# Performance work log

Hardware: AMD Instinct MI355X
Metric: run time of the kernel (lower is better)

Reference implementation:

```python
import jax, jax.numpy as jnp
import numpy as np

B, S1, S2, H, DW = 64, 512, 512, 768, 200


def setup_inputs() -> dict:
    key = jax.random.key(0)
    ks = jax.random.split(key, 16)
    inp = {
        'x1': jax.random.normal(ks[0], (B, S1, H), jnp.float32),
        'x1_h': jax.random.normal(ks[1], (B, H), jnp.float32),
        'x1_mask': jax.random.randint(ks[2], (B, S1), 0, 2, jnp.int32),
        'y': jax.random.normal(ks[3], (B, S1), jnp.float32),
        'x2': jax.random.normal(ks[4], (B, S2, H), jnp.float32),
        'x2_h': jax.random.normal(ks[5], (B, H), jnp.float32),
        'x2_mask': jax.random.randint(ks[6], (B, S2), 0, 2, jnp.int32),
        'tt': jax.random.normal(ks[7], (B, S1, DW), jnp.float32),
        'tt2': jax.random.normal(ks[8], (B, S2, DW), jnp.float32),
        # parameters (xavier ~ N(0, 2/(fan_in+fan_out)))
        'W_bert': jax.random.normal(ks[9], (H + 1, H), jnp.float32) * np.sqrt(2.0 / (H + 1 + H)),
        'W_wv': jax.random.normal(ks[10], (DW + 1, DW), jnp.float32) * np.sqrt(2.0 / (DW + 1 + DW)),
        'lin_wv_w': jax.random.normal(ks[11], (DW, H), jnp.float32) * np.sqrt(1.0 / DW),
        'lin_wv_b': jnp.zeros((H,), jnp.float32),
        'lin_w': jax.random.normal(ks[12], (4 * H, 1), jnp.float32) * np.sqrt(1.0 / (4 * H)),
        'lin_b': jnp.zeros((1,), jnp.float32),
    }
    return inp


def _branch(x_cat, W, keys_vals, x1_inv, x2_inv):
    # x_cat: [B,S1,D+1], W: [D+1,D], keys_vals: [B,S2,D]
    xw = jnp.matmul(x_cat, W)                                  # [B,S1,D]
    a = jnp.einsum('bsd,btd->bst', xw, keys_vals)              # [B,S1,S2]
    a = jnp.where(x2_inv[:, None, :], jnp.float32(-1e-5), a)   # faithful: tiny mask value, pre-softmax
    a = jax.nn.softmax(a, axis=-1)
    v = jnp.einsum('bst,btd->bsd', a, keys_vals)               # [B,S1,D]
    v = jnp.where(x1_inv[:, :, None], jnp.float32(-1e5), v)
    return v.max(axis=1)                                       # max-pool over S1 -> [B,D]


def reference(x1, x1_h, x1_mask, y, x2, x2_h, x2_mask, tt, tt2,
              W_bert, W_wv, lin_wv_w, lin_wv_b, lin_w, lin_b):
    x1_inv = (1 - x1_mask).astype(bool)  # True where padded
    x2_inv = (1 - x2_mask).astype(bool)

    # word-vector branch
    x1_wv = jnp.concatenate([tt, y[:, :, None]], axis=-1)      # [B,S1,201]
    x12_wv = _branch(x1_wv, W_wv, tt2, x1_inv, x2_inv)         # [B,200]
    x12_wv = x12_wv @ lin_wv_w + lin_wv_b                      # [B,768]

    # bert branch
    x1c = jnp.concatenate([x1, y[:, :, None]], axis=-1)        # [B,S1,769]
    x12 = _branch(x1c, W_bert, x2, x1_inv, x2_inv)             # [B,768]

    h = jnp.concatenate([x1_h, x2_h, x12, x12_wv], axis=1)     # [B,3072]
    o = jax.nn.sigmoid(h @ lin_w + lin_b)                      # [B,1]
    return (o, x1_inv.astype(jnp.int32), x2_inv.astype(jnp.int32))
```

## Files before the change

### kernel.cpp

```cpp
#include <hip/hip_runtime.h>


#define BB 64
#define SS 512
#define HH 768
#define DWW 200

typedef __attribute__((ext_vector_type(8))) _Float16 f16x8;
typedef __attribute__((ext_vector_type(4))) _Float16 f16x4;
typedef __attribute__((ext_vector_type(4))) float f32x4;
typedef unsigned int u32;

__device__ __forceinline__ u32 fkey(float f) {
    u32 u = __float_as_uint(f);
    return (u & 0x80000000u) ? ~u : (u | 0x80000000u);
}
__device__ __forceinline__ float fdec(u32 k) {
    u32 u = (k & 0x80000000u) ? (k & 0x7fffffffu) : ~k;
    return __uint_as_float(u);
}
__device__ __forceinline__ f32x4 mm(f16x8 a, f16x8 b, f32x4 c) {
    return __builtin_amdgcn_mfma_f32_16x16x32_f16(a, b, c, 0, 0, 0);
}
__device__ __forceinline__ void gl16(const void* g, void* l) {
    __builtin_amdgcn_global_load_lds(
        (const __attribute__((address_space(1))) void*)g,
        (__attribute__((address_space(3))) void*)l, 16, 0, 0);
}

__global__ __launch_bounds__(256) void k_setup(
    const int* __restrict__ m1, const int* __restrict__ m2,
    const float* __restrict__ Wb, const float* __restrict__ Wwv,
    float* __restrict__ out, u32* __restrict__ k1, u32* __restrict__ k2,
    int* __restrict__ idx1, int* __restrict__ rcnt1,
    int* __restrict__ idx2, int* __restrict__ rcnt2,
    _Float16* __restrict__ wbTH, _Float16* __restrict__ wwTH) {
    int bid = blockIdx.x, tid = threadIdx.x;
    if (bid < 128) {
        int i = bid * 256 + tid;
        out[BB + i]           = (float)(1 - m1[i]);
        out[BB + BB * SS + i] = (float)(1 - m2[i]);
    } else if (bid < 320) {
        int i = (bid - 128) * 256 + tid;
        u32 v = fkey(-1e5f);
        if (i < BB * HH) k1[i] = v;
        if (i < BB * DWW) k2[i] = v;
    } else if (bid < 448) {
        int b = (bid - 320) & 63;
        const int* m = (bid < 384) ? m1 : m2;
        int* idx = (bid < 384) ? idx1 : idx2;
        int* rcnt = (bid < 384) ? rcnt1 : rcnt2;
        if (tid < 64) {
            int base = 0;
#pragma unroll
            for (int c = 0; c < 8; ++c) {
                int s = c * 64 + tid;
                int v = m[b * SS + s];
                unsigned long long bal = __ballot(v != 0);
                int pre = __popcll(bal & ((1ull << tid) - 1ull));
                if (v) idx[b * SS + base + pre] = s;
                base += __popcll(bal);
            }
            if (tid == 0) rcnt[b] = base;
        }
    } else if (bid < 2848) {
        int i = (bid - 448) * 256 + tid;
        int n = i / 800, k = i - n * 800;
        wbTH[i] = (_Float16)((k < 769) ? Wb[(size_t)k * 768 + n] : 0.f);
    } else {
        int i = (bid - 2848) * 256 + tid;
        int n = i / 224, k = i - n * 224;
        wwTH[i] = (_Float16)((k < 201 && n < 200) ? Wwv[(size_t)k * 200 + n] : 0.f);
    }
}

__global__ __launch_bounds__(256) void k_prep(
    const float* __restrict__ x2, const float* __restrict__ tt2,
    const float* __restrict__ x1, const float* __restrict__ tt,
    const float* __restrict__ yv,
    const int* __restrict__ idx1, const int* __restrict__ rcnt1,
    const int* __restrict__ idx2, const int* __restrict__ rcnt2,
    _Float16* __restrict__ kvB, _Float16* __restrict__ kvTB,
    _Float16* __restrict__ kvW, _Float16* __restrict__ kvTW,
    _Float16* __restrict__ XcB, _Float16* __restrict__ XcW,
    int cb, int b0) {
    __shared__ float tile[64][65];
    int bx = blockIdx.x, tid = threadIdx.x;
    if (bx < cb * 128) {
        int cbi = bx >> 7, sub = bx & 127;
        int t0 = (sub & 7) * 64, ybr = sub >> 3;
        const float* src; _Float16* kv; _Float16* kvT; int D, DPAD, DTPAD, d0;
        if (ybr < 12) { src = x2;  kv = kvB; kvT = kvTB; D = 768; DPAD = 768; DTPAD = 768; d0 = ybr * 64; }
        else          { src = tt2; kv = kvW; kvT = kvTW; D = 200; DPAD = 256; DTPAD = 256; d0 = (ybr - 12) * 64; }
        int bg = b0 + cbi;
        int rc2 = rcnt2[bg];
        int tpad2 = (rc2 + 127) & ~127;
        if (t0 >= tpad2) return;
        int tq = tid >> 3, c8 = (tid & 7) * 8;
#pragma unroll
        for (int i = 0; i < 2; ++i) {
            int t = tq + i * 32;
            int tg = t0 + t;
            int gd = d0 + c8;
            float v[8] = {0.f, 0.f, 0.f, 0.f, 0.f, 0.f, 0.f, 0.f};
            if (tg < rc2) {
                int sg = idx2[bg * SS + tg];
                const float* rp = src + ((size_t)bg * SS + sg) * D + gd;
                if (gd + 7 < D) {
                    float4 p0 = *(const float4*)(rp);
                    float4 p1 = *(const float4*)(rp + 4);
                    v[0] = p0.x; v[1] = p0.y; v[2] = p0.z; v[3] = p0.w;
                    v[4] = p1.x; v[5] = p1.y; v[6] = p1.z; v[7] = p1.w;
                } else {
#pragma unroll
                    for (int j = 0; j < 8; ++j) {
                        int d = gd + j;
                        v[j] = (d < D) ? src[((size_t)bg * SS + sg) * D + d] : 0.f;
                    }
                }
            }
            f16x8 o;
#pragma unroll
            for (int j = 0; j < 8; ++j) {
                tile[t][c8 + j] = v[j];
                o[j] = (_Float16)v[j];
            }
            *(f16x8*)(kv + ((size_t)cbi * SS + tg) * DPAD + gd) = o;
        }
        __syncthreads();
#pragma unroll
        for (int i = 0; i < 2; ++i) {
            int dl = tq + i * 32, gdr = d0 + dl;
            if (gdr < DTPAD) {
                f16x8 o;
#pragma unroll
                for (int j = 0; j < 8; ++j) o[j] = (_Float16)tile[c8 + j][dl];
                *(f16x8*)(kvT + ((size_t)cbi * DTPAD + gdr) * SS + t0 + c8) = o;
            }
        }
    } else {
        bx -= cb * 128;
        int cbi = bx >> 8, xb = bx & 255;
        int bg = b0 + cbi;
        const float* X; _Float16* outp; int Din, KPAD; size_t ost;
        if (xb < 200) { X = x1; outp = XcB; Din = 768; KPAD = 800; ost = (size_t)cbi * 409600; }
        else { xb -= 200; X = tt; outp = XcW; Din = 200; KPAD = 224; ost = (size_t)cbi * 114688; }
        int i8 = (xb * 256 + tid) * 8;
        int s = i8 / KPAD, k0 = i8 - s * KPAD;
        int rc = rcnt1[bg];
        int rpad = (rc + 127) & ~127;
        if (s >= rpad) return;
        f16x8 o = {};
        if (s < rc) {
            int sg = idx1[bg * SS + s];
            const float* Xr = X + ((size_t)bg * SS + sg) * Din;
            if (k0 + 7 < Din) {
                float4 p0 = *(const float4*)(Xr + k0);
                float4 p1 = *(const float4*)(Xr + k0 + 4);
                o[0] = (_Float16)p0.x; o[1] = (_Float16)p0.y;
                o[2] = (_Float16)p0.z; o[3] = (_Float16)p0.w;
                o[4] = (_Float16)p1.x; o[5] = (_Float16)p1.y;
                o[6] = (_Float16)p1.z; o[7] = (_Float16)p1.w;
            } else {
#pragma unroll
                for (int j = 0; j < 8; ++j) {
                    int k = k0 + j;
                    float v = (k < Din) ? Xr[k]
                                        : ((k == Din) ? yv[(size_t)bg * SS + sg] : 0.f);
                    o[j] = (_Float16)v;
                }
            }
        }
        *(f16x8*)(outp + ost + (size_t)s * KPAD + k0) = o;
    }
}

template<int KA, int KST, int TN, int SXW, int DV, int AS, int BS, int EPI,
         bool GN, bool RK>
__device__ __forceinline__ void mm_core(
    const _Float16* __restrict__ A, const _Float16* __restrict__ B,
    _Float16* __restrict__ O, const float* __restrict__ rsum,
    u32* __restrict__ keys, int jb, const int* __restrict__ rcnt1,
    const int* __restrict__ rcnt2, int b0, char* lds, float* rsv) {
    int cbi = jb / (4 * TN);
    int rest = jb - cbi * (4 * TN);
    int ts = rest / TN, tn = rest - ts * TN;
    int s0 = ts * 128, n0 = tn * 128;

    int rc = rcnt1[b0 + cbi];
    int rpad = (rc + 127) & ~127;
    if (s0 >= rpad) return;
    if constexpr (GN) {
        int tp2 = (rcnt2[b0 + cbi] + 127) & ~127;
        if (n0 >= tp2) return;
    }

    int tid = threadIdx.x, lane = tid & 63, wid = tid >> 6;
    int wr = wid >> 1, wc = wid & 1;
    int l15 = lane & 15, sl = lane >> 4, gb = sl * 4;

    const _Float16* srcA = A + (size_t)cbi * AS + (size_t)s0 * KA;
    const _Float16* srcB = B + (size_t)cbi * BS + (size_t)n0 * KA;

    if constexpr (EPI == 2) {
        if (tid < 128) rsv[tid] = rsum[cbi * SS + s0 + tid];
    }

    f32x4 zz = {0.f, 0.f, 0.f, 0.f};
    f32x4 acc[4][4];
#pragma unroll
    for (int i = 0; i < 4; ++i)
#pragma unroll
        for (int j = 0; j < 4; ++j) acc[i][j] = zz;

#define STAGE(buf, ks)                                                        \
    _Pragma("unroll") for (int i = 0; i < 4; ++i) {                           \
        int c = wid + 4 * i;                                                  \
        int arr = c >> 3, sub = c & 7, slot = sub >> 1, rh = sub & 1;         \
        const _Float16* gp = (arr ? srcB : srcA) +                            \
            (size_t)(rh * 64 + lane) * KA + (ks) * 32 + slot * 8;             \
        gl16(gp, lds + (buf) * 16384 + c * 1024);                             \
    }
#define KBODY(ks, kend)                                                       \
    {                                                                         \
        if ((ks) + 1 < (kend)) STAGE(buf ^ 1, (ks) + 1);                      \
        char* base = lds + buf * 16384;                                       \
        f16x8 a[4], b[4];                                                     \
        _Pragma("unroll") for (int mf = 0; mf < 4; ++mf)                      \
            a[mf] = *(const f16x8*)(base + sl * 2048 +                        \
                                    (wr * 64 + mf * 16 + l15) * 16);          \
        _Pragma("unroll") for (int nf = 0; nf < 4; ++nf)                      \
            b[nf] = *(const f16x8*)(base + 8192 + sl * 2048 +                 \
                                    (wc * 64 + nf * 16 + l15) * 16);          \
        _Pragma("unroll") for (int mf = 0; mf < 4; ++mf)                      \
            _Pragma("unroll") for (int nf = 0; nf < 4; ++nf)                  \
                acc[mf][nf] = mm(a[mf], b[nf], acc[mf][nf]);                  \
        __syncthreads();                                                      \
        buf ^= 1;                                                             \
    }

    STAGE(0, 0);
    __syncthreads();
    int buf = 0;
    if constexpr (RK) {
        int kend = ((rcnt2[b0 + cbi] + 127) & ~127) >> 5;
        for (int ks = 0; ks < kend; ++ks) KBODY(ks, kend);
    } else {
#pragma unroll
        for (int ks = 0; ks < KST; ++ks) KBODY(ks, KST);
    }
#undef KBODY
#undef STAGE

    if constexpr (EPI == 1) {
        _Float16* ce = (_Float16*)lds;
#pragma unroll
        for (int mf = 0; mf < 4; ++mf)
#pragma unroll
            for (int nf = 0; nf < 4; ++nf)
#pragma unroll
                for (int r = 0; r < 4; ++r) {
                    int row = wr * 64 + mf * 16 + gb + r;
                    int col = wc * 64 + nf * 16 + l15;
                    ce[row * 128 + col] = (_Float16)acc[mf][nf][r];
                }
        __syncthreads();
#pragma unroll
        for (int i = 0; i < 8; ++i) {
            int t = tid + i * 256;
            int row = t >> 4, col = (t & 15) * 8;
            *(f16x8*)(O + ((size_t)cbi * SS + s0 + row) * SXW + n0 + col) =
                *(const f16x8*)(ce + row * 128 + col);
        }
    } else {
        int bg = b0 + cbi;
#pragma unroll
        for (int nf = 0; nf < 4; ++nf) {
            float mx = -3.0e38f;
#pragma unroll
            for (int mf = 0; mf < 4; ++mf)
#pragma unroll
                for (int r = 0; r < 4; ++r) {
                    int srow = wr * 64 + mf * 16 + gb + r;
                    if (s0 + srow < rc) mx = fmaxf(mx, acc[mf][nf][r] * rsv[srow]);
                }
            mx = fmaxf(mx, __shfl_xor(mx, 16));
            mx = fmaxf(mx, __shfl_xor(mx, 32));
            if (lane < 16) {
                int d = n0 + wc * 64 + nf * 16 + lane;
                if (d < DV) atomicMax(&keys[(size_t)bg * DV + d], fkey(mx));
            }
        }
    }
}

template<int EPI, bool GN, bool RK,
         int KA0, int KST0, int TN0, int SXW0, int DV0, int AS0, int BS0,
         int KA1, int KST1, int TN1, int SXW1, int DV1, int AS1, int BS1>
__global__ __launch_bounds__(256) void k_mmM(
    const _Float16* __restrict__ A0, const _Float16* __restrict__ B0,
    _Float16* __restrict__ O0, const float* __restrict__ rs0, u32* __restrict__ key0,
    const _Float16* __restrict__ A1, const _Float16* __restrict__ B1,
    _Float16* __restrict__ O1, const float* __restrict__ rs1, u32* __restrict__ key1,
    int nj0, const int* __restrict__ rcnt1, const int* __restrict__ rcnt2,
    int b0, int nwg) {
    __shared__ __align__(16) char lds[32768];
    __shared__ float rsv[128];
    int bid = blockIdx.x;
    int x = bid & 7, t = bid >> 3;
    int tb = nj0 >> 3;
    int tw = (nwg - nj0) >> 3;
    if (t < tb)
        mm_core<KA0, KST0, TN0, SXW0, DV0, AS0, BS0, EPI, GN, RK>(
            A0, B0, O0, rs0, key0, x * tb + t, rcnt1, rcnt2, b0, lds, rsv);
    else
        mm_core<KA1, KST1, TN1, SXW1, DV1, AS1, BS1, EPI, GN, RK>(
            A1, B1, O1, rs1, key1, x * tw + (t - tb), rcnt1, rcnt2, b0, lds, rsv);
}

__global__ __launch_bounds__(256) void k_softmaxM(
    _Float16* __restrict__ SP0, float* __restrict__ rs0,
    _Float16* __restrict__ SP1, float* __restrict__ rs1,
    const int* __restrict__ rcnt1, const int* __restrict__ rcnt2,
    int nblk0, int b0) {
    int bid = blockIdx.x;
    bool selw = bid >= nblk0;
    int b = selw ? bid - nblk0 : bid;
    _Float16* SP = selw ? SP1 : SP0;
    float* rs = selw ? rs1 : rs0;
    int cbi = b >> 7, rb = b & 127;
    int wid = threadIdx.x >> 6, lane = threadIdx.x & 63;
    int row = rb * 4 + wid, bg = b0 + cbi;
    int rc1 = rcnt1[bg];
    if (row >= rc1) return;
    int rc2 = rcnt2[bg];
    int col0 = lane * 8;
    f16x8 sv = *(const f16x8*)(SP + ((size_t)cbi * SS + row) * SS + col0);
    float mx = -3.0e38f;
    float c[8];
#pragma unroll
    for (int j = 0; j < 8; ++j) {
        c[j] = (float)sv[j];
        if (col0 + j < rc2) mx = fmaxf(mx, c[j]);
    }
#pragma unroll
    for (int off = 1; off <= 32; off <<= 1) mx = fmaxf(mx, __shfl_xor(mx, off));
    f16x8 o;
    float sm = 0.f;
#pragma unroll
    for (int j = 0; j < 8; ++j) {
        _Float16 h = (col0 + j < rc2) ? (_Float16)__expf(c[j] - mx) : (_Float16)0.f;
        o[j] = h;
        sm += (float)h;
    }
#pragma unroll
    for (int off = 1; off <= 32; off <<= 1) sm += __shfl_xor(sm, off);
    *(f16x8*)(SP + ((size_t)cbi * SS + row) * SS + col0) = o;
    if (lane == 0) rs[cbi * SS + row] = 1.0f / sm;
}

__global__ __launch_bounds__(256) void k_tail(
    const float* __restrict__ x1h, const float* __restrict__ x2h,
    const u32* __restrict__ keys, const u32* __restrict__ wvkeys,
    const float* __restrict__ Wp, const float* __restrict__ bp,
    const float* __restrict__ lw, const float* __restrict__ lb,
    float* __restrict__ out) {
    int b = blockIdx.x, tid = threadIdx.x;
    __shared__ float xv[DWW];
    __shared__ float wvp[HH];
    __shared__ float red[4];
    if (tid < DWW) xv[tid] = fdec(wvkeys[b * DWW + tid]);
    __syncthreads();
    for (int h = tid; h < HH; h += 256) {
        float acc = bp[h];
        for (int d = 0; d < DWW; ++d) acc += xv[d] * Wp[d * HH + h];
        wvp[h] = acc;
    }
    __syncthreads();
    float acc = 0.f;
    for (int i = tid; i < HH; i += 256) {
        acc += x1h[b * HH + i] * lw[i];
        acc += x2h[b * HH + i] * lw[HH + i];
        acc += fdec(keys[b * HH + i]) * lw[2 * HH + i];
        acc += wvp[i] * lw[3 * HH + i];
    }
    int wid = tid >> 6, lane = tid & 63;
#pragma unroll
    for (int off = 32; off; off >>= 1) acc += __shfl_down(acc, off);
    if (lane == 0) red[wid] = acc;
    __syncthreads();
    if (tid == 0) {
        float z = red[0] + red[1] + red[2] + red[3] + lb[0];
        out[b] = 1.f / (1.f + __expf(-z));
    }
}

extern "C" void kernel_launch(void* const* d_in, const int* in_sizes, int n_in,
                              void* d_out, int out_size, void* d_ws, size_t ws_size,
                              hipStream_t stream) {
    const float* x1   = (const float*)d_in[0];
    const float* x1h  = (const float*)d_in[1];
    const int*   m1   = (const int*)d_in[2];
    const float* y    = (const float*)d_in[3];
    const float* x2   = (const float*)d_in[4];
    const float* x2h  = (const float*)d_in[5];
    const int*   m2   = (const int*)d_in[6];
    const float* tt   = (const float*)d_in[7];
    const float* tt2  = (const float*)d_in[8];
    const float* Wb   = (const float*)d_in[9];
    const float* Wwv  = (const float*)d_in[10];
    const float* lwvw = (const float*)d_in[11];
    const float* lwvb = (const float*)d_in[12];
    const float* lw   = (const float*)d_in[13];
    const float* lb   = (const float*)d_in[14];
    float* out = (float*)d_out;
    char* ws = (char*)d_ws;

    u32*      x12key   = (u32*)ws;
    u32*      x12wvkey = (u32*)(ws + 196608);
    float*    rsumB    = (float*)(ws + 444416);
    float*    rsumW    = (float*)(ws + 575488);
    _Float16* wbTH     = (_Float16*)(ws + 706560);
    _Float16* wwTH     = (_Float16*)(ws + 1935360);
    int*      idx1Buf  = (int*)(ws + 2050048);
    int*      rcnt1Buf = (int*)(ws + 2181120);
    int*      idx2Buf  = (int*)(ws + 2181376);
    int*      rcnt2Buf = (int*)(ws + 2312448);
    const size_t D0 = 2312704;

    k_setup<<<3072, 256, 0, stream>>>(m1, m2, Wb, Wwv, out, x12key, x12wvkey,
                                      idx1Buf, rcnt1Buf, idx2Buf, rcnt2Buf,
                                      wbTH, wwTH);

    const size_t perb = 4194304;
    int nb = 1;
    if (ws_size > D0 + perb) nb = (int)((ws_size - D0) / perb);
    if (nb > BB) nb = BB;
    if (nb < 1) nb = 1;

    char* R = ws + D0;
    _Float16* XcB = (_Float16*)R;
    _Float16* XcW = (_Float16*)(R + (size_t)nb * 819200);
    _Float16* S_b = (_Float16*)R;
    _Float16* S_w = (_Float16*)(R + (size_t)nb * 524288);
    char* p = R + (size_t)nb * 1048576;
    _Float16* XW_b = (_Float16*)p; p += (size_t)nb * 786432;
    _Float16* XW_w = (_Float16*)p; p += (size_t)nb * 262144;
    _Float16* KV_b = (_Float16*)p; p += (size_t)nb * 786432;
    _Float16* KV_w = (_Float16*)p; p += (size_t)nb * 262144;
    _Float16* KT_b = (_Float16*)p; p += (size_t)nb * 786432;
    _Float16* KT_w = (_Float16*)p;

    for (int b0 = 0; b0 < BB; b0 += nb) {
        int cb = (BB - b0 < nb) ? (BB - b0) : nb;
        k_prep<<<cb * 384, 256, 0, stream>>>(
            x2, tt2, x1, tt, y, idx1Buf, rcnt1Buf, idx2Buf, rcnt2Buf,
            KV_b, KT_b, KV_w, KT_w, XcB, XcW, cb, b0);
        k_mmM<1, false, false,
              800, 25, 6, 768, 0, 409600, 0,
              224,  7, 2, 256, 0, 114688, 0><<<cb * 32, 256, 0, stream>>>(
            XcB, wbTH, XW_b, nullptr, nullptr,
            XcW, wwTH, XW_w, nullptr, nullptr,
            cb * 24, rcnt1Buf, rcnt2Buf, b0, cb * 32);
        k_mmM<1, true, false,
              768, 24, 4, 512, 0, 393216, 393216,
              256,  8, 4, 512, 0, 131072, 131072><<<cb * 32, 256, 0, stream>>>(
            XW_b, KV_b, S_b, nullptr, nullptr,
            XW_w, KV_w, S_w, nullptr, nullptr,
            cb * 16, rcnt1Buf, rcnt2Buf, b0, cb * 32);
        k_softmaxM<<<cb * 256, 256, 0, stream>>>(
            S_b, rsumB, S_w, rsumW, rcnt1Buf, rcnt2Buf, cb * 128, b0);
        k_mmM<2, false, true,
              512, 16, 6, 0, 768, 262144, 393216,
              512, 16, 2, 0, 200, 262144, 131072><<<cb * 32, 256, 0, stream>>>(
            S_b, KT_b, nullptr, rsumB, x12key,
            S_w, KT_w, nullptr, rsumW, x12wvkey,
            cb * 24, rcnt1Buf, rcnt2Buf, b0, cb * 32);
    }

    k_tail<<<BB, 256, 0, stream>>>(x1h, x2h, x12key, x12wvkey,
                                   lwvw, lwvb, lw, lb, out);
}
```

Before: 271.4 us.

## Fold weight transpose and output init into prep kernel; trim PV K-loop

The setup kernel is reduced to only the mask compaction (one wave per batch row). Output mask writes, max-key initialisation and the f16 weight transposes move into extra blocks of the first prep launch, and the transposes now write 4 halves per thread. The RK K-loop now stops at the true key count rounded to 32 instead of 128, skipping zero-padded key chunks. This saves a large standalone launch and overlaps the weight conversion with the KV/X preparation. The cost is a more complex prep kernel whose weight blocks only run in the first batch chunk.

```diff
diff --git a/kernel.cpp b/kernel.cpp
--- a/kernel.cpp
+++ b/kernel.cpp
@@ -28,65 +28,47 @@
         (__attribute__((address_space(3))) void*)l, 16, 0, 0);
 }
 
-__global__ __launch_bounds__(256) void k_setup(
+__global__ __launch_bounds__(64) void k_setup(
     const int* __restrict__ m1, const int* __restrict__ m2,
-    const float* __restrict__ Wb, const float* __restrict__ Wwv,
-    float* __restrict__ out, u32* __restrict__ k1, u32* __restrict__ k2,
     int* __restrict__ idx1, int* __restrict__ rcnt1,
-    int* __restrict__ idx2, int* __restrict__ rcnt2,
-    _Float16* __restrict__ wbTH, _Float16* __restrict__ wwTH) {
-    int bid = blockIdx.x, tid = threadIdx.x;
-    if (bid < 128) {
-        int i = bid * 256 + tid;
-        out[BB + i]           = (float)(1 - m1[i]);
-        out[BB + BB * SS + i] = (float)(1 - m2[i]);
-    } else if (bid < 320) {
-        int i = (bid - 128) * 256 + tid;
-        u32 v = fkey(-1e5f);
-        if (i < BB * HH) k1[i] = v;
-        if (i < BB * DWW) k2[i] = v;
-    } else if (bid < 448) {
-        int b = (bid - 320) & 63;
-        const int* m = (bid < 384) ? m1 : m2;
-        int* idx = (bid < 384) ? idx1 : idx2;
-        int* rcnt = (bid < 384) ? rcnt1 : rcnt2;
-        if (tid < 64) {
-            int base = 0;
-#pragma unroll
-            for (int c = 0; c < 8; ++c) {
-                int s = c * 64 + tid;
-                int v = m[b * SS + s];
-                unsigned long long bal = __ballot(v != 0);
-                int pre = __popcll(bal & ((1ull << tid) - 1ull));
-                if (v) idx[b * SS + base + pre] = s;
-                base += __popcll(bal);
-            }
-            if (tid == 0) rcnt[b] = base;
-        }
-    } else if (bid < 2848) {
-        int i = (bid - 448) * 256 + tid;
-        int n = i / 800, k = i - n * 800;
-        wbTH[i] = (_Float16)((k < 769) ? Wb[(size_t)k * 768 + n] : 0.f);
-    } else {
-        int i = (bid - 2848) * 256 + tid;
-        int n = i / 224, k = i - n * 224;
-        wwTH[i] = (_Float16)((k < 201 && n < 200) ? Wwv[(size_t)k * 200 + n] : 0.f);
-    }
+    int* __restrict__ idx2, int* __restrict__ rcnt2) {
+    int bid = blockIdx.x, lane = threadIdx.x;
+    int b = bid & 63;
+    const int* m = (bid < 64) ? m1 : m2;
+    int* idx = (bid < 64) ? idx1 : idx2;
+    int* rcnt = (bid < 64) ? rcnt1 : rcnt2;
+    int base = 0;
+#pragma unroll
+    for (int c = 0; c < 8; ++c) {
+        int s = c * 64 + lane;
+        int v = m[b * SS + s];
+        unsigned long long bal = __ballot(v != 0);
+        int pre = __popcll(bal & ((1ull << lane) - 1ull));
+        if (v) idx[b * SS + base + pre] = s;
+        base += __popcll(bal);
+    }
+    if (lane == 0) rcnt[b] = base;
 }
 
 __global__ __launch_bounds__(256) void k_prep(
     const float* __restrict__ x2, const float* __restrict__ tt2,
     const float* __restrict__ x1, const float* __restrict__ tt,
     const float* __restrict__ yv,
+    const int* __restrict__ m1, const int* __restrict__ m2,
+    const float* __restrict__ Wb, const float* __restrict__ Wwv,
     const int* __restrict__ idx1, const int* __restrict__ rcnt1,
     const int* __restrict__ idx2, const int* __restrict__ rcnt2,
     _Float16* __restrict__ kvB, _Float16* __restrict__ kvTB,
     _Float16* __restrict__ kvW, _Float16* __restrict__ kvTW,
     _Float16* __restrict__ XcB, _Float16* __restrict__ XcW,
+    float* __restrict__ out, u32* __restrict__ k1, u32* __restrict__ k2,
+    _Float16* __restrict__ wbTH, _Float16* __restrict__ wwTH,
     int cb, int b0) {
     __shared__ float tile[64][65];
     int bx = blockIdx.x, tid = threadIdx.x;
-    if (bx < cb * 128) {
+    int NKV = cb * 128, NXC = cb * 256;
+
+    if (bx < NKV) {
         int cbi = bx >> 7, sub = bx & 127;
         int t0 = (sub & 7) * 64, ybr = sub >> 3;
         const float* src; _Float16* kv; _Float16* kvT; int D, DPAD, DTPAD, d0;
@@ -138,9 +120,9 @@
                 *(f16x8*)(kvT + ((size_t)cbi * DTPAD + gdr) * SS + t0 + c8) = o;
             }
         }
-    } else {
-        bx -= cb * 128;
-        int cbi = bx >> 8, xb = bx & 255;
+    } else if (bx < NKV + NXC) {
+        int u = bx - NKV;
+        int cbi = u >> 8, xb = u & 255;
         int bg = b0 + cbi;
         const float* X; _Float16* outp; int Din, KPAD; size_t ost;
         if (xb < 200) { X = x1; outp = XcB; Din = 768; KPAD = 800; ost = (size_t)cbi * 409600; }
@@ -172,6 +154,34 @@
             }
         }
         *(f16x8*)(outp + ost + (size_t)s * KPAD + k0) = o;
+    } else {
+        int u = bx - NKV - NXC;
+        if (u < 128) {
+            int i = u * 256 + tid;
+            out[BB + i]           = (float)(1 - m1[i]);
+            out[BB + BB * SS + i] = (float)(1 - m2[i]);
+        } else if (u < 320) {
+            int i = (u - 128) * 256 + tid;
+            u32 v = fkey(-1e5f);
+            if (i < BB * HH) k1[i] = v;
+            if (i < BB * DWW) k2[i] = v;
+        } else if (u < 920) {
+            int i = ((u - 320) * 256 + tid) * 4;
+            int n = i / 800, k = i - n * 800;
+            f16x4 o;
+#pragma unroll
+            for (int j = 0; j < 4; ++j)
+                o[j] = (_Float16)((k + j < 769) ? Wb[(size_t)(k + j) * 768 + n] : 0.f);
+            *(f16x4*)(wbTH + i) = o;
+        } else {
+            int i = ((u - 920) * 256 + tid) * 4;
+            int n = i / 224, k = i - n * 224;
+            f16x4 o;
+#pragma unroll
+            for (int j = 0; j < 4; ++j)
+                o[j] = (_Float16)((k + j < 201 && n < 200) ? Wwv[(size_t)(k + j) * 200 + n] : 0.f);
+            *(f16x4*)(wwTH + i) = o;
+        }
     }
 }
 
@@ -243,7 +253,7 @@
     __syncthreads();
     int buf = 0;
     if constexpr (RK) {
-        int kend = ((rcnt2[b0 + cbi] + 127) & ~127) >> 5;
+        int kend = (rcnt2[b0 + cbi] + 31) >> 5;
         for (int ks = 0; ks < kend; ++ks) KBODY(ks, kend);
     } else {
 #pragma unroll
@@ -428,9 +438,7 @@
     int*      rcnt2Buf = (int*)(ws + 2312448);
     const size_t D0 = 2312704;
 
-    k_setup<<<3072, 256, 0, stream>>>(m1, m2, Wb, Wwv, out, x12key, x12wvkey,
-                                      idx1Buf, rcnt1Buf, idx2Buf, rcnt2Buf,
-                                      wbTH, wwTH);
+    k_setup<<<128, 64, 0, stream>>>(m1, m2, idx1Buf, rcnt1Buf, idx2Buf, rcnt2Buf);
 
     const size_t perb = 4194304;
     int nb = 1;
@@ -453,9 +461,12 @@
 
     for (int b0 = 0; b0 < BB; b0 += nb) {
         int cb = (BB - b0 < nb) ? (BB - b0) : nb;
-        k_prep<<<cb * 384, 256, 0, stream>>>(
-            x2, tt2, x1, tt, y, idx1Buf, rcnt1Buf, idx2Buf, rcnt2Buf,
-            KV_b, KT_b, KV_w, KT_w, XcB, XcW, cb, b0);
+        int nprep = cb * 384 + ((b0 == 0) ? 976 : 0);
+        k_prep<<<nprep, 256, 0, stream>>>(
+            x2, tt2, x1, tt, y, m1, m2, Wb, Wwv,
+            idx1Buf, rcnt1Buf, idx2Buf, rcnt2Buf,
+            KV_b, KT_b, KV_w, KT_w, XcB, XcW,
+            out, x12key, x12wvkey, wbTH, wwTH, cb, b0);
         k_mmM<1, false, false,
               800, 25, 6, 768, 0, 409600, 0,
               224,  7, 2, 256, 0, 114688, 0><<<cb * 32, 256, 0, stream>>>(
```

New measurement: 270.0 us. Within noise of the previous version (-0.5%).
